# Kernel optimization log

Measured on AMD Instinct MI355X. Metric: run time of the kernel, lower is better.

The kernel has to match this reference:

```python
import jax, jax.numpy as jnp
import numpy as np

D_MODEL = 1024
N_HEADS = 16
HEAD_DIM = D_MODEL // N_HEADS
NEG_INF = -1e10  # masked_fill value used in the original


def setup_inputs() -> dict:
    key = jax.random.key(0)
    ks = jax.random.split(key, 12)
    B, L = 2, 2048
    s = 0.02
    return {
        "query": jax.random.normal(ks[0], (B, L, D_MODEL), jnp.float32),
        "key": jax.random.normal(ks[1], (B, L, D_MODEL), jnp.float32),
        "value": jax.random.normal(ks[2], (B, L, D_MODEL), jnp.float32),
        "mask": jnp.ones((B, 1, L, L), jnp.int32),
        "Wq": jax.random.normal(ks[3], (D_MODEL, D_MODEL), jnp.float32) * s,
        "bq": jax.random.normal(ks[4], (D_MODEL,), jnp.float32) * s,
        "Wk": jax.random.normal(ks[5], (D_MODEL, D_MODEL), jnp.float32) * s,
        "bk": jax.random.normal(ks[6], (D_MODEL,), jnp.float32) * s,
        "Wv": jax.random.normal(ks[7], (D_MODEL, D_MODEL), jnp.float32) * s,
        "bv": jax.random.normal(ks[8], (D_MODEL,), jnp.float32) * s,
        "Wo": jax.random.normal(ks[9], (D_MODEL, D_MODEL), jnp.float32) * s,
        "bo": jax.random.normal(ks[10], (D_MODEL,), jnp.float32) * s,
    }


def _split_heads(x, B):
    # [B, L, D] -> [B, H, L, hd]
    return x.reshape(B, -1, N_HEADS, HEAD_DIM).transpose(0, 2, 1, 3)


def reference(query, key, value, mask, Wq, bq, Wk, bk, Wv, bv, Wo, bo):
    B = query.shape[0]
    scale = jnp.sqrt(jnp.asarray(HEAD_DIM, query.dtype))
    Q = _split_heads(query @ Wq + bq, B)   # [B,H,Lq,hd]
    K = _split_heads(key @ Wk + bk, B)     # [B,H,Lk,hd]
    V = _split_heads(value @ Wv + bv, B)   # [B,H,Lk,hd]
    energy = jnp.einsum('bhqd,bhkd->bhqk', Q, K) / scale
    energy = jnp.where(mask == 0, jnp.asarray(NEG_INF, energy.dtype), energy)
    # NOTE: the original applies softmax over dim=1 (the HEADS axis); replicated faithfully.
    attention = jax.nn.softmax(energy, axis=1)
    x = jnp.einsum('bhqk,bhkd->bhqd', attention, V)  # dropout is identity at inference
    x = x.transpose(0, 2, 1, 3).reshape(B, -1, D_MODEL)
    return x @ Wo + bo
```

## Files before the change

kernel.cpp:

```cpp
#include <hip/hip_runtime.h>
#include <hip/hip_bf16.h>
#include <stdint.h>

#define DM 1024
#define NH 16
#define HD 64
#define SEQ 2048
#define NB 2

typedef __attribute__((ext_vector_type(8)))  __bf16 bf16x8;
typedef __attribute__((ext_vector_type(4)))  __bf16 bf16x4;
typedef __attribute__((ext_vector_type(4)))  float  f32x4;
typedef __attribute__((ext_vector_type(16))) float  f32x16;
typedef __attribute__((ext_vector_type(4)))  unsigned int uint4v;
typedef __attribute__((ext_vector_type(4)))  int    i32x4;

__device__ __forceinline__ f32x16 mfma32x32(bf16x8 a, bf16x8 b, f32x16 c) {
  return __builtin_amdgcn_mfma_f32_32x32x16_bf16(a, b, c, 0, 0, 0);
}
__device__ __forceinline__ f32x4 mfma16x16(bf16x8 a, bf16x8 b, f32x4 c) {
  return __builtin_amdgcn_mfma_f32_16x16x32_bf16(a, b, c, 0, 0, 0);
}
__device__ __forceinline__ unsigned pkbf(float a, float b) {
  unsigned short ua = __builtin_bit_cast(unsigned short, (__bf16)a);
  unsigned short ub = __builtin_bit_cast(unsigned short, (__bf16)b);
  return (unsigned)ua | ((unsigned)ub << 16);
}
__device__ __forceinline__ f32x16 zero16() {
  f32x16 z;
#pragma unroll
  for (int i = 0; i < 16; i++) z[i] = 0.0f;
  return z;
}

__global__ void wconv_kernel(const float* __restrict__ Wq, const float* __restrict__ Wk,
                             const float* __restrict__ Wv, const float* __restrict__ Wo,
                             __bf16* __restrict__ Wt) {
  __shared__ float tile[32][33];
  const int which = blockIdx.z;
  const float* W = (which == 0) ? Wq : (which == 1) ? Wk : (which == 2) ? Wv : Wo;
  __bf16* out = Wt + (size_t)which * DM * DM;
  const int n0 = blockIdx.x * 32, k0 = blockIdx.y * 32;
  const int tx = threadIdx.x & 31, ty = threadIdx.x >> 5;
#pragma unroll
  for (int i = 0; i < 4; i++) {
    tile[ty + i * 8][tx] = W[(size_t)(k0 + ty + i * 8) * DM + n0 + tx];
  }
  __syncthreads();
#pragma unroll
  for (int i = 0; i < 4; i++) {
    out[(size_t)(n0 + ty + i * 8) * DM + k0 + tx] = (__bf16)tile[tx][ty + i * 8];
  }
}

__global__ __launch_bounds__(256, 3)
void qkv_kernel(const float* __restrict__ Aq, const float* __restrict__ Ak,
                const float* __restrict__ Av, const __bf16* __restrict__ Wt,
                const float* __restrict__ bqv, const float* __restrict__ bkv,
                const float* __restrict__ bvv, __bf16* __restrict__ Qh,
                __bf16* __restrict__ Kh, __bf16* __restrict__ Vt) {
  __shared__ __bf16 Alds[128][40];
  __shared__ __bf16 Blds[128][40];
  const int z = blockIdx.z;
  const float* A = (z == 0) ? Aq : (z == 1) ? Ak : Av;
  const __bf16* Bt = Wt + (size_t)z * DM * DM;
  const float* bias = (z == 0) ? bqv : (z == 1) ? bkv : bvv;

  const int tid = threadIdx.x;
  const int l = tid & 63, w = tid >> 6;
  const int wm = w >> 1, wn = w & 1;
  const int r0 = blockIdx.x * 128, c0 = blockIdx.y * 128;

  f32x4 acc[4][4];
#pragma unroll
  for (int m = 0; m < 4; m++)
#pragma unroll
    for (int n = 0; n < 4; n++)
#pragma unroll
      for (int r = 0; r < 4; r++) acc[m][n][r] = 0.0f;

  const int ar = tid >> 2;
  const int aq = tid & 3;
  const int br = tid >> 1;
  const int bh = tid & 1;

  for (int kt = 0; kt < DM / 32; kt++) {
#pragma unroll
    for (int rep = 0; rep < 2; rep++) {
      const int row = ar + rep * 64;
      const float* src = A + (size_t)(r0 + row) * DM + kt * 32 + aq * 8;
      const f32x4 v0 = *(const f32x4*)(src);
      const f32x4 v1 = *(const f32x4*)(src + 4);
      bf16x8 av;
#pragma unroll
      for (int i = 0; i < 4; i++) { av[i] = (__bf16)v0[i]; av[4 + i] = (__bf16)v1[i]; }
      *(bf16x8*)&Alds[row][aq * 8] = av;
    }
    {
      const __bf16* bsrc = Bt + (size_t)(c0 + br) * DM + kt * 32 + bh * 16;
      bf16x8 v0 = *(const bf16x8*)bsrc;
      bf16x8 v1 = *(const bf16x8*)(bsrc + 8);
      *(bf16x8*)&Blds[br][bh * 16] = v0;
      *(bf16x8*)&Blds[br][bh * 16 + 8] = v1;
    }
    __syncthreads();
    bf16x8 af[4], bfr[4];
#pragma unroll
    for (int m = 0; m < 4; m++)
      af[m] = *(const bf16x8*)&Alds[wm * 64 + m * 16 + (l & 15)][(l >> 4) * 8];
#pragma unroll
    for (int n = 0; n < 4; n++)
      bfr[n] = *(const bf16x8*)&Blds[wn * 64 + n * 16 + (l & 15)][(l >> 4) * 8];
#pragma unroll
    for (int m = 0; m < 4; m++)
#pragma unroll
      for (int n = 0; n < 4; n++) acc[m][n] = mfma16x16(af[m], bfr[n], acc[m][n]);
    __syncthreads();
  }

  const int ccol = l & 15;
  const int crb = (l >> 4) * 4;
  __bf16* Ohm = (z == 0) ? Qh : Kh;
#pragma unroll
  for (int n = 0; n < 4; n++) {
    const int col = c0 + wn * 64 + n * 16 + ccol;
    const float bv = bias[col];
    const int h = col >> 6, d = col & 63;
#pragma unroll
    for (int m = 0; m < 4; m++) {
      const int row = r0 + wm * 64 + m * 16 + crb;
      f32x4 v = acc[m][n];
#pragma unroll
      for (int r = 0; r < 4; r++) v[r] += bv;
      if (z < 2) {
#pragma unroll
        for (int r = 0; r < 4; r++) {
          const int rr = row + r; const int bb = rr >> 11; const int ll = rr & 2047;
          Ohm[(((size_t)bb * NH + h) * SEQ + ll) * HD + d] = (__bf16)v[r];
        }
      } else {
        const int bb = row >> 11, ll = row & 2047;
        bf16x4 pk;
#pragma unroll
        for (int r = 0; r < 4; r++) pk[r] = (__bf16)v[r];
        *(bf16x4*)&Vt[(((size_t)bb * NH + h) * HD + d) * SEQ + ll] = pk;
      }
    }
  }
}

__global__ __launch_bounds__(512, 2)
void denom_kernel(const __bf16* __restrict__ Qh, const __bf16* __restrict__ Kh,
                  const int* __restrict__ mask, __bf16* __restrict__ Dinv,
                  unsigned* __restrict__ mbit) {
  const int tid = threadIdx.x;
  const int l = tid & 63, w = tid >> 6;
  const int lq = l & 31, hi = l >> 5;
  const int ktg = blockIdx.x;
  const int b = blockIdx.y;
  const int qt = blockIdx.z;
  const int q0 = qt * 32;
  const int k0 = (ktg * 8 + w) * 32;

  unsigned word = 0;
  {
    const i32x4* mp = (const i32x4*)(mask + ((size_t)b * SEQ + q0 + lq) * SEQ + k0);
#pragma unroll
    for (int j = 0; j < 8; j++) {
      const i32x4 v = mp[j];
      word |= (v.x ? 1u : 0u) << (4 * j);
      word |= (v.y ? 1u : 0u) << (4 * j + 1);
      word |= (v.z ? 1u : 0u) << (4 * j + 2);
      word |= (v.w ? 1u : 0u) << (4 * j + 3);
    }
    if (hi == 0) mbit[((size_t)b * SEQ + q0 + lq) * (SEQ / 32) + (k0 >> 5)] = word;
  }

  float dsum[16];
#pragma unroll
  for (int r = 0; r < 16; r++) dsum[r] = 0.0f;

  const __bf16* qbase = Qh + ((size_t)b * NH) * SEQ * HD + (size_t)(q0 + lq) * HD + hi * 8;
  const __bf16* kbase = Kh + ((size_t)b * NH) * SEQ * HD + (size_t)(k0 + lq) * HD + hi * 8;

  for (int h = 0; h < NH; h++) {
    const __bf16* qp = qbase + (size_t)h * SEQ * HD;
    const __bf16* kp = kbase + (size_t)h * SEQ * HD;
    bf16x8 qf[4], kf[4];
#pragma unroll
    for (int ch = 0; ch < 4; ch++) {
      qf[ch] = *(const bf16x8*)(qp + ch * 16);
      kf[ch] = *(const bf16x8*)(kp + ch * 16);
    }
    f32x16 e = zero16();
#pragma unroll
    for (int ch = 0; ch < 4; ch++) e = mfma32x32(kf[ch], qf[ch], e);
#pragma unroll
    for (int r = 0; r < 16; r++) {
      const int crow = (r & 3) + 8 * (r >> 2) + 4 * hi;
      const float bv = ((word >> crow) & 1u) ? 0.0f : -1e10f;
      dsum[r] += __expf(fmaf(e[r], 0.125f, bv));
    }
  }
#pragma unroll
  for (int r = 0; r < 16; r++) {
    const int crow = (r & 3) + 8 * (r >> 2) + 4 * hi;
    Dinv[((size_t)b * SEQ + k0 + crow) * SEQ + q0 + lq] =
        (__bf16)__builtin_amdgcn_rcpf(dsum[r]);
  }
}

__global__ __launch_bounds__(256, 2)
void attn2_kernel(const __bf16* __restrict__ Qh, const __bf16* __restrict__ Kh,
                  const __bf16* __restrict__ Vt, const __bf16* __restrict__ Dinv,
                  const unsigned* __restrict__ mbit, __bf16* __restrict__ X) {
  const int tid = threadIdx.x;
  const int l = tid & 63, w = tid >> 6;
  const int lq = l & 31, hi = l >> 5;
  const int bh = blockIdx.x;
  const int b = bh >> 4;
  const int q0 = (blockIdx.y * 4 + w) * 32;

  bf16x8 qf[4];
  {
    const __bf16* qp = Qh + ((size_t)bh * SEQ + q0 + lq) * HD + hi * 8;
#pragma unroll
    for (int ch = 0; ch < 4; ch++) qf[ch] = *(const bf16x8*)(qp + ch * 16);
  }
  f32x16 x0 = zero16(), x1 = zero16();

  const __bf16* kbase = Kh + (size_t)bh * SEQ * HD;
  const __bf16* vbase = Vt + (size_t)bh * HD * SEQ;
  const unsigned* mrow = mbit + ((size_t)b * SEQ + q0 + lq) * (SEQ / 32);
  const __bf16* drow = Dinv + (size_t)b * SEQ * SEQ + q0 + lq;

  for (int kt = 0; kt < SEQ / 32; kt++) {
    const int k0 = kt * 32;
    f32x16 e = zero16();
#pragma unroll
    for (int ch = 0; ch < 4; ch++) {
      const bf16x8 kf = *(const bf16x8*)(kbase + (size_t)(k0 + lq) * HD + ch * 16 + hi * 8);
      e = mfma32x32(kf, qf[ch], e);
    }
    const unsigned word = mrow[kt];
    float p[16], rd[16];
#pragma unroll
    for (int r = 0; r < 16; r++) {
      const int crow = (r & 3) + 8 * (r >> 2) + 4 * hi;
      const float bv = ((word >> crow) & 1u) ? 0.0f : -1e10f;
      p[r] = __expf(fmaf(e[r], 0.125f, bv));
      rd[r] = (float)drow[(size_t)(k0 + crow) * SEQ];
    }
    unsigned u[8];
#pragma unroll
    for (int j = 0; j < 8; j++) {
      const float a = p[2 * j] * rd[2 * j];
      const float bb2 = p[2 * j + 1] * rd[2 * j + 1];
      u[j] = pkbf(a, bb2);
    }
    unsigned t[8];
#pragma unroll
    for (int j = 0; j < 8; j++) t[j] = (unsigned)__shfl_xor((int)u[j], 32, 64);
    const unsigned w0 = hi ? t[2] : u[0];
    const unsigned w1 = hi ? t[3] : u[1];
    const unsigned w2 = hi ? u[2] : t[0];
    const unsigned w3 = hi ? u[3] : t[1];
    const unsigned w4 = hi ? t[6] : u[4];
    const unsigned w5 = hi ? t[7] : u[5];
    const unsigned w6 = hi ? u[6] : t[4];
    const unsigned w7 = hi ? u[7] : t[5];
    const uint4v s0v = {w0, w1, w2, w3};
    const uint4v s1v = {w4, w5, w6, w7};
    const bf16x8 pa0 = __builtin_bit_cast(bf16x8, s0v);
    const bf16x8 pa1 = __builtin_bit_cast(bf16x8, s1v);
    const __bf16* vp = vbase + (size_t)lq * SEQ + k0 + hi * 8;
    bf16x8 vf;
    vf = *(const bf16x8*)(vp);                         x0 = mfma32x32(pa0, vf, x0);
    vf = *(const bf16x8*)(vp + 16);                    x0 = mfma32x32(pa1, vf, x0);
    vf = *(const bf16x8*)(vp + (size_t)32 * SEQ);      x1 = mfma32x32(pa0, vf, x1);
    vf = *(const bf16x8*)(vp + (size_t)32 * SEQ + 16); x1 = mfma32x32(pa1, vf, x1);
  }

  __bf16* xo = X + ((size_t)bh * SEQ + q0) * HD;
#pragma unroll
  for (int dt = 0; dt < 2; dt++) {
    const f32x16& xx = dt ? x1 : x0;
#pragma unroll
    for (int r = 0; r < 16; r++) {
      const int crow = (r & 3) + 8 * (r >> 2) + 4 * hi;
      xo[(size_t)crow * HD + dt * 32 + lq] = (__bf16)xx[r];
    }
  }
}

__global__ __launch_bounds__(256, 4)
void ogemm_kernel(const __bf16* __restrict__ X, const __bf16* __restrict__ Bt,
                  const float* __restrict__ bias, float* __restrict__ Out) {
  __shared__ __bf16 Alds[64][40];
  __shared__ __bf16 Blds[128][40];
  const int tid = threadIdx.x;
  const int l = tid & 63, w = tid >> 6;
  const int r0 = blockIdx.x * 64, c0 = blockIdx.y * 128;

  f32x4 acc[4][2];
#pragma unroll
  for (int m = 0; m < 4; m++)
#pragma unroll
    for (int n = 0; n < 2; n++)
#pragma unroll
      for (int r = 0; r < 4; r++) acc[m][n][r] = 0.0f;

  const int ar = tid >> 2, aq = tid & 3;
  const int br = tid >> 1, bh = tid & 1;
  const int rr = r0 + ar;
  const int bb = rr >> 11, ll = rr & 2047;

  for (int kt = 0; kt < DM / 32; kt++) {
    {
      const int cc = kt * 32 + aq * 8;
      const int h = cc >> 6, d = cc & 63;
      const size_t off = (((size_t)bb * NH + h) * SEQ + ll) * HD + d;
      *(bf16x8*)&Alds[ar][aq * 8] = *(const bf16x8*)(X + off);
    }
    {
      const __bf16* bsrc = Bt + (size_t)(c0 + br) * DM + kt * 32 + bh * 16;
      bf16x8 v0 = *(const bf16x8*)bsrc;
      bf16x8 v1 = *(const bf16x8*)(bsrc + 8);
      *(bf16x8*)&Blds[br][bh * 16] = v0;
      *(bf16x8*)&Blds[br][bh * 16 + 8] = v1;
    }
    __syncthreads();
    bf16x8 af[4], bfr[2];
#pragma unroll
    for (int m = 0; m < 4; m++)
      af[m] = *(const bf16x8*)&Alds[m * 16 + (l & 15)][(l >> 4) * 8];
#pragma unroll
    for (int n = 0; n < 2; n++)
      bfr[n] = *(const bf16x8*)&Blds[w * 32 + n * 16 + (l & 15)][(l >> 4) * 8];
#pragma unroll
    for (int m = 0; m < 4; m++)
#pragma unroll
      for (int n = 0; n < 2; n++) acc[m][n] = mfma16x16(af[m], bfr[n], acc[m][n]);
    __syncthreads();
  }

  const int ccol = l & 15;
  const int crb = (l >> 4) * 4;
#pragma unroll
  for (int n = 0; n < 2; n++) {
    const int col = c0 + w * 32 + n * 16 + ccol;
    const float bv = bias[col];
#pragma unroll
    for (int m = 0; m < 4; m++) {
      const int row = r0 + m * 16 + crb;
      f32x4 v = acc[m][n];
#pragma unroll
      for (int r = 0; r < 4; r++) Out[(size_t)(row + r) * DM + col] = v[r] + bv;
    }
  }
}

extern "C" void kernel_launch(void* const* d_in, const int* in_sizes, int n_in,
                              void* d_out, int out_size, void* d_ws, size_t ws_size,
                              hipStream_t stream) {
  const float* q = (const float*)d_in[0];
  const float* k = (const float*)d_in[1];
  const float* v = (const float*)d_in[2];
  const int* msk = (const int*)d_in[3];
  const float* Wq = (const float*)d_in[4];
  const float* bq = (const float*)d_in[5];
  const float* Wk = (const float*)d_in[6];
  const float* bk = (const float*)d_in[7];
  const float* Wv = (const float*)d_in[8];
  const float* bv = (const float*)d_in[9];
  const float* Wo = (const float*)d_in[10];
  const float* bo = (const float*)d_in[11];

  char* ws = (char*)d_ws;
  const size_t MB = 1024 * 1024;
  if (ws_size < 64 * MB) return;
  __bf16* Wt = (__bf16*)(ws);
  __bf16* Qh = (__bf16*)(ws + 8 * MB);
  __bf16* Kh = (__bf16*)(ws + 16 * MB);
  __bf16* Vt = (__bf16*)(ws + 24 * MB);
  __bf16* X  = (__bf16*)(ws + 32 * MB);
  __bf16* Dinv = (__bf16*)(ws + 40 * MB);
  unsigned* mbit = (unsigned*)(ws + 57 * MB);

  wconv_kernel<<<dim3(32, 32, 4), 256, 0, stream>>>(Wq, Wk, Wv, Wo, Wt);
  qkv_kernel<<<dim3(32, 8, 3), 256, 0, stream>>>(q, k, v, Wt, bq, bk, bv, Qh, Kh, Vt);
  denom_kernel<<<dim3(8, 2, 64), 512, 0, stream>>>(Qh, Kh, msk, Dinv, mbit);
  attn2_kernel<<<dim3(32, 16), 256, 0, stream>>>(Qh, Kh, Vt, Dinv, mbit, X);
  ogemm_kernel<<<dim3(64, 8), 256, 0, stream>>>(X, Wt + (size_t)3 * DM * DM, bo, (float*)d_out);
}
```

Before: 511.3 us.

## Split attention key loop across grid, transpose Dinv layout, reduce partials in ogemm

The attention kernel's key loop is split into NC=2 chunks across a new grid dimension. Each chunk writes a partial output buffer, and the output GEMM sums the partials in fp32 when it loads its A tile. Dinv is now stored query-major so attn2 can load it as contiguous bf16x8 vectors instead of strided scalar loads, and the denom kernel writes it in packed bf16x4 stores. Launch bounds raise occupancy hints, and the workspace is rearranged, with Wo moved to slot 0. The cost is extra traffic for the partial buffers and an added bf16 rounding step per partial.

```diff
diff --git a/kernel.cpp b/kernel.cpp
--- a/kernel.cpp
+++ b/kernel.cpp
@@ -7,6 +7,7 @@
 #define HD 64
 #define SEQ 2048
 #define NB 2
+#define NC 2
 
 typedef __attribute__((ext_vector_type(8)))  __bf16 bf16x8;
 typedef __attribute__((ext_vector_type(4)))  __bf16 bf16x4;
@@ -39,7 +40,7 @@
   __shared__ float tile[32][33];
   const int which = blockIdx.z;
   const float* W = (which == 0) ? Wq : (which == 1) ? Wk : (which == 2) ? Wv : Wo;
-  __bf16* out = Wt + (size_t)which * DM * DM;
+  __bf16* out = Wt + (size_t)((which + 1) & 3) * DM * DM;
   const int n0 = blockIdx.x * 32, k0 = blockIdx.y * 32;
   const int tx = threadIdx.x & 31, ty = threadIdx.x >> 5;
 #pragma unroll
@@ -63,7 +64,7 @@
   __shared__ __bf16 Blds[128][40];
   const int z = blockIdx.z;
   const float* A = (z == 0) ? Aq : (z == 1) ? Ak : Av;
-  const __bf16* Bt = Wt + (size_t)z * DM * DM;
+  const __bf16* Bt = Wt + (size_t)(z + 1) * DM * DM;
   const float* bias = (z == 0) ? bqv : (z == 1) ? bkv : bvv;
 
   const int tid = threadIdx.x;
@@ -149,7 +150,7 @@
   }
 }
 
-__global__ __launch_bounds__(512, 2)
+__global__ __launch_bounds__(512, 4)
 void denom_kernel(const __bf16* __restrict__ Qh, const __bf16* __restrict__ Kh,
                   const int* __restrict__ mask, __bf16* __restrict__ Dinv,
                   unsigned* __restrict__ mbit) {
@@ -202,24 +203,28 @@
       dsum[r] += __expf(fmaf(e[r], 0.125f, bv));
     }
   }
-#pragma unroll
-  for (int r = 0; r < 16; r++) {
-    const int crow = (r & 3) + 8 * (r >> 2) + 4 * hi;
-    Dinv[((size_t)b * SEQ + k0 + crow) * SEQ + q0 + lq] =
-        (__bf16)__builtin_amdgcn_rcpf(dsum[r]);
-  }
-}
-
-__global__ __launch_bounds__(256, 2)
+  const size_t qrow = ((size_t)b * SEQ + q0 + lq) * SEQ;
+#pragma unroll
+  for (int g = 0; g < 4; g++) {
+    bf16x4 pk;
+#pragma unroll
+    for (int j = 0; j < 4; j++)
+      pk[j] = (__bf16)__builtin_amdgcn_rcpf(dsum[g * 4 + j]);
+    *(bf16x4*)&Dinv[qrow + k0 + 8 * g + 4 * hi] = pk;
+  }
+}
+
+__global__ __launch_bounds__(256, 4)
 void attn2_kernel(const __bf16* __restrict__ Qh, const __bf16* __restrict__ Kh,
                   const __bf16* __restrict__ Vt, const __bf16* __restrict__ Dinv,
-                  const unsigned* __restrict__ mbit, __bf16* __restrict__ X) {
+                  const unsigned* __restrict__ mbit, __bf16* __restrict__ Xp) {
   const int tid = threadIdx.x;
   const int l = tid & 63, w = tid >> 6;
   const int lq = l & 31, hi = l >> 5;
   const int bh = blockIdx.x;
   const int b = bh >> 4;
   const int q0 = (blockIdx.y * 4 + w) * 32;
+  const int c = blockIdx.z;
 
   bf16x8 qf[4];
   {
@@ -232,9 +237,9 @@
   const __bf16* kbase = Kh + (size_t)bh * SEQ * HD;
   const __bf16* vbase = Vt + (size_t)bh * HD * SEQ;
   const unsigned* mrow = mbit + ((size_t)b * SEQ + q0 + lq) * (SEQ / 32);
-  const __bf16* drow = Dinv + (size_t)b * SEQ * SEQ + q0 + lq;
-
-  for (int kt = 0; kt < SEQ / 32; kt++) {
+  const __bf16* drow = Dinv + ((size_t)b * SEQ + q0 + lq) * SEQ;
+
+  for (int kt = c * (SEQ / 32 / NC); kt < (c + 1) * (SEQ / 32 / NC); kt++) {
     const int k0 = kt * 32;
     f32x16 e = zero16();
 #pragma unroll
@@ -242,14 +247,20 @@
       const bf16x8 kf = *(const bf16x8*)(kbase + (size_t)(k0 + lq) * HD + ch * 16 + hi * 8);
       e = mfma32x32(kf, qf[ch], e);
     }
+    bf16x8 dv[4];
+#pragma unroll
+    for (int g = 0; g < 4; g++) dv[g] = *(const bf16x8*)(drow + k0 + 8 * g);
     const unsigned word = mrow[kt];
     float p[16], rd[16];
 #pragma unroll
     for (int r = 0; r < 16; r++) {
-      const int crow = (r & 3) + 8 * (r >> 2) + 4 * hi;
+      const int j = r & 3, g = r >> 2;
+      const int crow = j + 8 * g + 4 * hi;
       const float bv = ((word >> crow) & 1u) ? 0.0f : -1e10f;
       p[r] = __expf(fmaf(e[r], 0.125f, bv));
-      rd[r] = (float)drow[(size_t)(k0 + crow) * SEQ];
+      const float rlo = (float)dv[g][j];
+      const float rhi = (float)dv[g][j + 4];
+      rd[r] = hi ? rhi : rlo;
     }
     unsigned u[8];
 #pragma unroll
@@ -281,7 +292,8 @@
     vf = *(const bf16x8*)(vp + (size_t)32 * SEQ + 16); x1 = mfma32x32(pa1, vf, x1);
   }
 
-  __bf16* xo = X + ((size_t)bh * SEQ + q0) * HD;
+  const size_t XCH = (size_t)NB * NH * SEQ * HD;
+  __bf16* xo = Xp + (size_t)c * XCH + ((size_t)bh * SEQ + q0) * HD;
 #pragma unroll
   for (int dt = 0; dt < 2; dt++) {
     const f32x16& xx = dt ? x1 : x0;
@@ -294,7 +306,7 @@
 }
 
 __global__ __launch_bounds__(256, 4)
-void ogemm_kernel(const __bf16* __restrict__ X, const __bf16* __restrict__ Bt,
+void ogemm_kernel(const __bf16* __restrict__ Xp, const __bf16* __restrict__ Bt,
                   const float* __restrict__ bias, float* __restrict__ Out) {
   __shared__ __bf16 Alds[64][40];
   __shared__ __bf16 Blds[128][40];
@@ -312,6 +324,7 @@
 
   const int ar = tid >> 2, aq = tid & 3;
   const int br = tid >> 1, bh = tid & 1;
+  const size_t PART = (size_t)NB * NH * SEQ * HD;
   const int rr = r0 + ar;
   const int bb = rr >> 11, ll = rr & 2047;
 
@@ -320,7 +333,19 @@
       const int cc = kt * 32 + aq * 8;
       const int h = cc >> 6, d = cc & 63;
       const size_t off = (((size_t)bb * NH + h) * SEQ + ll) * HD + d;
-      *(bf16x8*)&Alds[ar][aq * 8] = *(const bf16x8*)(X + off);
+      float fv[8];
+#pragma unroll
+      for (int i = 0; i < 8; i++) fv[i] = 0.0f;
+#pragma unroll
+      for (int c = 0; c < NC; c++) {
+        const bf16x8 v = *(const bf16x8*)(Xp + (size_t)c * PART + off);
+#pragma unroll
+        for (int i = 0; i < 8; i++) fv[i] += (float)v[i];
+      }
+      bf16x8 av;
+#pragma unroll
+      for (int i = 0; i < 8; i++) av[i] = (__bf16)fv[i];
+      *(bf16x8*)&Alds[ar][aq * 8] = av;
     }
     {
       const __bf16* bsrc = Bt + (size_t)(c0 + br) * DM + kt * 32 + bh * 16;
@@ -380,16 +405,16 @@
   const size_t MB = 1024 * 1024;
   if (ws_size < 64 * MB) return;
   __bf16* Wt = (__bf16*)(ws);
+  unsigned* mbit = (unsigned*)(ws + 2 * MB);
   __bf16* Qh = (__bf16*)(ws + 8 * MB);
   __bf16* Kh = (__bf16*)(ws + 16 * MB);
   __bf16* Vt = (__bf16*)(ws + 24 * MB);
-  __bf16* X  = (__bf16*)(ws + 32 * MB);
-  __bf16* Dinv = (__bf16*)(ws + 40 * MB);
-  unsigned* mbit = (unsigned*)(ws + 57 * MB);
+  __bf16* Xp = (__bf16*)(ws + 32 * MB);
+  __bf16* Dinv = (__bf16*)(ws + 48 * MB);
 
   wconv_kernel<<<dim3(32, 32, 4), 256, 0, stream>>>(Wq, Wk, Wv, Wo, Wt);
   qkv_kernel<<<dim3(32, 8, 3), 256, 0, stream>>>(q, k, v, Wt, bq, bk, bv, Qh, Kh, Vt);
   denom_kernel<<<dim3(8, 2, 64), 512, 0, stream>>>(Qh, Kh, msk, Dinv, mbit);
-  attn2_kernel<<<dim3(32, 16), 256, 0, stream>>>(Qh, Kh, Vt, Dinv, mbit, X);
-  ogemm_kernel<<<dim3(64, 8), 256, 0, stream>>>(X, Wt + (size_t)3 * DM * DM, bo, (float*)d_out);
-}
+  attn2_kernel<<<dim3(32, 16, NC), 256, 0, stream>>>(Qh, Kh, Vt, Dinv, mbit, Xp);
+  ogemm_kernel<<<dim3(64, 8), 256, 0, stream>>>(Xp, Wt, bo, (float*)d_out);
+}
```

Result: slower. 536.1 us (+4.8%).
